# Performance work log

Measured on AMD Instinct MI355X. Metric: run time of the kernel, lower is better.

## Reference

```python
import jax, jax.numpy as jnp
import numpy as np

NUM_EMBEDDINGS = 4096
EMBEDDING_DIM = 256


def setup_inputs() -> dict:
    key = jax.random.key(0)
    k1, k2 = jax.random.split(key)
    # x: [B, C, H, W] latent feature map, C == embedding_dim
    x = jax.random.normal(k1, (4, EMBEDDING_DIM, 64, 64), dtype=jnp.float32)
    # codebook initialized uniform(-1/K, 1/K) as in the torch module
    emb = jax.random.uniform(
        k2, (NUM_EMBEDDINGS, EMBEDDING_DIM), dtype=jnp.float32,
        minval=-1.0 / NUM_EMBEDDINGS, maxval=1.0 / NUM_EMBEDDINGS)
    return {"x": x, "emb": emb}


def reference(x, emb):
    # x: [B, C, H, W] -> x_flat: [B, L, C] with L = H*W
    B, C = x.shape[0], x.shape[1]
    x_flat = x.reshape(B, C, -1).transpose(0, 2, 1)
    x_sq = jnp.sum(x_flat * x_flat, axis=2, keepdims=True)      # [B, L, 1]
    e_sq = jnp.sum(emb * emb, axis=1)                            # [K]
    dots = jnp.einsum('blc,kc->blk', x_flat, emb)                # [B, L, K]
    distances = x_sq + e_sq - 2.0 * dots
    closest_indices = jnp.argmin(distances, axis=2)              # [B, L]
    return closest_indices, distances
```

## Files before the change

### kernel.cpp

```cpp
#include <hip/hip_runtime.h>
#include <hip/hip_fp16.h>

#define BB 4
#define CC 256
#define LL 4096
#define MM 16384
#define KK 4096
#define MARGIN 1.0e-4f

typedef _Float16 half8 __attribute__((ext_vector_type(8)));
typedef _Float16 half4_ __attribute__((ext_vector_type(4)));
typedef float f32x4 __attribute__((ext_vector_type(4)));

#define GLOAD16(gp, lp) __builtin_amdgcn_global_load_lds( \
    (const __attribute__((address_space(1))) void*)(gp),  \
    (__attribute__((address_space(3))) void*)(lp), 16, 0, 0)

__global__ void vq_prep(const float* __restrict__ x, const float* __restrict__ emb,
                        _Float16* __restrict__ xh, float* __restrict__ xsq,
                        _Float16* __restrict__ eh, float* __restrict__ esq) {
  __shared__ float tl[32][260];
  const int t = threadIdx.x;
  if (blockIdx.x < 512) {
    const int b = blockIdx.x >> 7, l0 = (blockIdx.x & 127) * 32;
    const float* src = x + (size_t)b * CC * LL + l0;
#pragma unroll
    for (int it = 0; it < 32; ++it) {
      const int idx = it * 256 + t;
      const int c = idx >> 5, l = idx & 31;
      tl[l][c] = src[(size_t)c * LL + l];
    }
    __syncthreads();
#pragma unroll
    for (int it = 0; it < 4; ++it) {
      const int u = it * 256 + t;
      const int l = u >> 5, c8 = (u & 31) * 8;
      half8 h;
#pragma unroll
      for (int j = 0; j < 8; ++j) h[j] = (_Float16)tl[l][c8 + j];
      *(half8*)(xh + ((size_t)(b * LL + l0 + l)) * CC + c8) = h;
    }
    if (t < 32) {
      float S[2];
#pragma unroll
      for (int blk = 0; blk < 2; ++blk) {
        float v[16];
#pragma unroll
        for (int ln = 0; ln < 16; ++ln) {
          float q[8];
#pragma unroll
          for (int j = 0; j < 8; ++j) {
            const float xv = tl[t][blk * 128 + j * 16 + ln];
            q[j] = xv * xv;
          }
          v[ln] = ((q[0] + q[1]) + (q[2] + q[3])) + ((q[4] + q[5]) + (q[6] + q[7]));
        }
        float s1[8], s2[4], s3[2];
#pragma unroll
        for (int ln = 0; ln < 8; ++ln) s1[ln] = v[ln] + v[ln + 8];
#pragma unroll
        for (int ln = 0; ln < 4; ++ln) s2[ln] = s1[ln] + s1[ln + 4];
#pragma unroll
        for (int ln = 0; ln < 2; ++ln) s3[ln] = s2[ln] + s2[ln + 2];
        S[blk] = s3[0] + s3[1];
      }
      xsq[b * LL + l0 + t] = S[0] + S[1];
    }
  } else {
    const int lane = t & 63, w = t >> 6;
    const int q = (blockIdx.x - 512) * 4 + w;
    const float4 v = ((const float4*)(emb + (size_t)q * CC))[lane];
    float vv[4] = {v.x, v.y, v.z, v.w};
    _Float16 h[4];
#pragma unroll
    for (int i = 0; i < 4; ++i) h[i] = (_Float16)(vv[i] * 4096.0f);
    *(half4_*)(eh + (size_t)q * CC + lane * 4) = half4_{h[0], h[1], h[2], h[3]};
    if (lane == 0) {
      const float* pe = emb + (size_t)q * CC;
      float S[2];
#pragma unroll
      for (int blk = 0; blk < 2; ++blk) {
        float vt[16];
#pragma unroll
        for (int ln = 0; ln < 16; ++ln) {
          float qq[8];
#pragma unroll
          for (int j = 0; j < 8; ++j) {
            const float ev = pe[blk * 128 + j * 16 + ln];
            qq[j] = ev * ev;
          }
          vt[ln] = ((qq[0] + qq[1]) + (qq[2] + qq[3])) + ((qq[4] + qq[5]) + (qq[6] + qq[7]));
        }
        float s1[8], s2[4], s3[2];
#pragma unroll
        for (int ln = 0; ln < 8; ++ln) s1[ln] = vt[ln] + vt[ln + 8];
#pragma unroll
        for (int ln = 0; ln < 4; ++ln) s2[ln] = s1[ln] + s1[ln + 4];
#pragma unroll
        for (int ln = 0; ln < 2; ++ln) s3[ln] = s2[ln] + s2[ln + 2];
        S[blk] = s3[0] + s3[1];
      }
      esq[q] = S[0] + S[1];
    }
  }
}

__global__ __launch_bounds__(256) void vq_gemm(
    const _Float16* __restrict__ xh, const _Float16* __restrict__ eh,
    const float* __restrict__ xsq, const float* __restrict__ esq,
    float* __restrict__ out,
    float* __restrict__ ps1, int* __restrict__ pi1, float* __restrict__ ps2) {
  __shared__ __align__(16) char smem[49152];
  float* sOut = (float*)smem;

  const int t = threadIdx.x, lane = t & 63, wid = t >> 6;
  const int wm = wid >> 1, wn = wid & 1;
  const int m0 = blockIdx.x * 128, n0 = blockIdx.y * 128;
  const int lm = lane & 15, kb = lane >> 4;

  const int srow = lane >> 2;
  const int scol = (((lane & 3) ^ (srow & 3)) * 8);
  const int chunk0 = wid * 2, chunk1 = wid * 2 + 1;
  const int row0 = chunk0 * 16 + srow, row1 = chunk1 * 16 + srow;
  const int rg = (kb ^ (lm & 3)) * 8;

  float ev[4], xs4[4][4];
#pragma unroll
  for (int ni = 0; ni < 4; ++ni) ev[ni] = esq[n0 + wn * 64 + ni * 16 + lm];
#pragma unroll
  for (int mi = 0; mi < 4; ++mi)
#pragma unroll
    for (int r = 0; r < 4; ++r)
      xs4[mi][r] = xsq[m0 + wm * 64 + mi * 16 + kb * 4 + r];
  __builtin_amdgcn_sched_barrier(0);

#define SA(b) ((_Float16*)(smem + (b) * 16384))
#define SB(b) ((_Float16*)(smem + (b) * 16384 + 8192))
#define STAGE(ks, buf) do {                                                   \
    const int kc_ = (ks) * 32 + scol;                                         \
    GLOAD16(xh + (size_t)(m0 + row0) * CC + kc_, SA(buf) + chunk0 * 512);     \
    GLOAD16(eh + (size_t)(n0 + row0) * CC + kc_, SB(buf) + chunk0 * 512);     \
    GLOAD16(xh + (size_t)(m0 + row1) * CC + kc_, SA(buf) + chunk1 * 512);     \
    GLOAD16(eh + (size_t)(n0 + row1) * CC + kc_, SB(buf) + chunk1 * 512);     \
  } while (0)

  f32x4 acc[4][4] = {};
  STAGE(0, 0);
  STAGE(1, 1);
#pragma unroll
  for (int ks = 0; ks < 8; ++ks) {
    const int cur = ks % 3;
    if (ks < 7) {
      asm volatile("s_waitcnt vmcnt(4) lgkmcnt(0)" ::: "memory");
    } else {
      asm volatile("s_waitcnt vmcnt(0) lgkmcnt(0)" ::: "memory");
    }
    __builtin_amdgcn_s_barrier();
    __builtin_amdgcn_sched_barrier(0);

    if (ks < 6) STAGE(ks + 2, (ks + 2) % 3);

    half8 a[4], bfr[4];
#pragma unroll
    for (int i = 0; i < 4; ++i) {
      a[i]   = *(const half8*)&SA(cur)[(wm * 64 + i * 16 + lm) * 32 + rg];
      bfr[i] = *(const half8*)&SB(cur)[(wn * 64 + i * 16 + lm) * 32 + rg];
    }
#pragma unroll
    for (int mi = 0; mi < 4; ++mi)
#pragma unroll
      for (int ni = 0; ni < 4; ++ni)
        acc[mi][ni] = __builtin_amdgcn_mfma_f32_16x16x32_f16(a[mi], bfr[ni], acc[mi][ni], 0, 0, 0);
  }
#undef STAGE

#define EPI_BAR() do {                                          \
    asm volatile("s_waitcnt lgkmcnt(0)" ::: "memory");          \
    __builtin_amdgcn_s_barrier();                               \
    __builtin_amdgcn_sched_barrier(0);                          \
  } while (0)

  const int swz = kb << 4;
  const int erow = t >> 3, ej = t & 7;
  const int esw = ((erow >> 2) & 3) << 4;
  const int egm0 = m0 + (erow >> 4) * 64 + (erow & 15);

#pragma unroll
  for (int mi = 0; mi < 4; ++mi) {
#pragma unroll
    for (int r = 0; r < 4; ++r) {
      const int row = wm * 16 + kb * 4 + r;
#pragma unroll
      for (int ni = 0; ni < 4; ++ni) {
        float t1 = xs4[mi][r] + ev[ni];
        float d = t1 - acc[mi][ni][r] * 4.8828125e-4f;
        sOut[row * 128 + ((wn * 64 + ni * 16 + lm) ^ swz)] = d;
      }
    }
    EPI_BAR();
    float s1 = 3.4e38f, s2 = 3.4e38f;
    int q1 = 0x7fffffff;
    const int gm = egm0 + mi * 16;
#pragma unroll
    for (int i = 0; i < 4; ++i) {
      const int c = 4 * ej + 32 * i;
      const f32x4 v = *(const f32x4*)&sOut[erow * 128 + (c ^ esw)];
      __builtin_nontemporal_store(v, (f32x4*)(out + MM + (size_t)gm * (size_t)KK + n0 + c));
#pragma unroll
      for (int e = 0; e < 4; ++e) {
        const float d = v[e];
        const int q = n0 + c + e;
        if (d < s1 || (d == s1 && q < q1)) { s2 = s1; s1 = d; q1 = q; }
        else s2 = fminf(s2, d);
      }
    }
#pragma unroll
    for (int off = 1; off < 8; off <<= 1) {
      float o1 = __shfl_xor(s1, off), o2 = __shfl_xor(s2, off);
      int oq = __shfl_xor(q1, off);
      float mx = fmaxf(s1, o1);
      if (o1 < s1 || (o1 == s1 && oq < q1)) { s1 = o1; q1 = oq; }
      s2 = fminf(fminf(s2, o2), mx);
    }
    if (ej == 0) {
      const size_t pidx = (size_t)gm * 32 + blockIdx.y;
      ps1[pidx] = s1; pi1[pidx] = q1; ps2[pidx] = s2;
    }
    if (mi < 3) EPI_BAR();
  }
#undef EPI_BAR
#undef SA
#undef SB
}

__global__ void vq_finish(const float* __restrict__ ps1, const int* __restrict__ pi1,
                          const float* __restrict__ ps2, const float* __restrict__ dist,
                          const float* __restrict__ x, const float* __restrict__ emb,
                          const float* __restrict__ xsq, const float* __restrict__ esq,
                          float* __restrict__ out) {
  __shared__ float xr[4][CC];
  __shared__ int cq[4][64];
  __shared__ int cnt[4];
  const int lane = threadIdx.x & 63, w = threadIdx.x >> 6;
  const int m = blockIdx.x * 4 + w;

  float s1 = 3.4e38f, s2 = 3.4e38f;
  int q1 = 0x7fffffff;
  if (lane < 32) {
    const size_t base = (size_t)m * 32 + lane;
    s1 = ps1[base]; s2 = ps2[base]; q1 = pi1[base];
  }
#pragma unroll
  for (int off = 1; off < 32; off <<= 1) {
    float o1 = __shfl_xor(s1, off), o2 = __shfl_xor(s2, off);
    int oq = __shfl_xor(q1, off);
    float mx = fmaxf(s1, o1);
    if (o1 < s1 || (o1 == s1 && oq < q1)) { s1 = o1; q1 = oq; }
    s2 = fminf(fminf(s2, o2), mx);
  }
  s1 = __shfl(s1, 0); s2 = __shfl(s2, 0); q1 = __shfl(q1, 0);

  if (s2 - s1 > MARGIN) {
    if (lane == 0) out[m] = (float)q1;
    return;
  }

  const int b = m >> 12, l = m & 4095;
#pragma unroll
  for (int j = 0; j < 4; ++j)
    xr[w][lane * 4 + j] = x[((size_t)b * CC + lane * 4 + j) * LL + l];
  if (lane == 0) cnt[w] = 0;

  const float thr = s1 + MARGIN;
  const float4* d4 = (const float4*)(dist + (size_t)m * KK);
  for (int i = 0; i < 16; ++i) {
    float4 v = d4[i * 64 + lane];
    float vv[4] = {v.x, v.y, v.z, v.w};
#pragma unroll
    for (int e = 0; e < 4; ++e)
      if (vv[e] <= thr) {
        int slot = atomicAdd(&cnt[w], 1);
        if (slot < 64) cq[w][slot] = (i * 64 + lane) * 4 + e;
      }
  }
  const int nc = min(cnt[w], 64);
  float bs = 3.4e38f;
  int bq = 0x7fffffff;
  if (lane < nc) {
    const int q = cq[w][lane];
    const float* e = emb + (size_t)q * CC;
    float a = 0.f;
    for (int c = 0; c < CC; ++c) a = fmaf(xr[w][c], e[c], a);
    float t1 = xsq[m] + esq[q];
    bs = t1 - 2.0f * a;
    bq = q;
  }
#pragma unroll
  for (int off = 1; off < 64; off <<= 1) {
    float os = __shfl_xor(bs, off);
    int oq = __shfl_xor(bq, off);
    if (os < bs || (os == bs && oq < bq)) { bs = os; bq = oq; }
  }
  if (lane == 0) out[m] = (float)bq;
}

extern "C" void kernel_launch(void* const* d_in, const int* in_sizes, int n_in,
                              void* d_out, int out_size, void* d_ws, size_t ws_size,
                              hipStream_t stream) {
  const float* x = (const float*)d_in[0];
  const float* emb = (const float*)d_in[1];
  float* out = (float*)d_out;
  char* ws = (char*)d_ws;

  _Float16* xh = (_Float16*)(ws + 0);
  _Float16* eh = (_Float16*)(ws + 8388608);
  float* xsq = (float*)(ws + 10485760);
  float* esq = (float*)(ws + 10551296);
  float* ps1 = (float*)(ws + 10567680);
  int*   pi1 = (int*)(ws + 12664832);
  float* ps2 = (float*)(ws + 14761984);

  vq_prep<<<1536, 256, 0, stream>>>(x, emb, xh, xsq, eh, esq);
  vq_gemm<<<dim3(128, 32), 256, 0, stream>>>(xh, eh, xsq, esq, out, ps1, pi1, ps2);
  vq_finish<<<4096, 256, 0, stream>>>(ps1, pi1, ps2, out + MM, x, emb, xsq, esq, out);
}
```

Baseline: 127.4 us.

## Use per-wave LDS slices in GEMM epilogue to remove block barriers

The epilogue now has each wave stage its own 64x64 output quadrant in a private LDS slice, in two 32-row chunks. This replaces the block-wide tile that needed an s_barrier for every 16-row group. Each wave writes its distance rows and reduces top-2 minima over 64 columns, so the number of partial results per row doubles from 32 to 64. The finish kernel reads and reduces 64 partials per row with a full-wave shuffle reduction. This removes cross-wave synchronization, at the cost of more partial-result traffic and a longer shuffle chain.

```diff
diff --git a/kernel.cpp b/kernel.cpp
--- a/kernel.cpp
+++ b/kernel.cpp
@@ -111,7 +111,6 @@
     float* __restrict__ out,
     float* __restrict__ ps1, int* __restrict__ pi1, float* __restrict__ ps2) {
   __shared__ __align__(16) char smem[49152];
-  float* sOut = (float*)smem;
 
   const int t = threadIdx.x, lane = t & 63, wid = t >> 6;
   const int wm = wid >> 1, wn = wid & 1;
@@ -174,61 +173,66 @@
   }
 #undef STAGE
 
-#define EPI_BAR() do {                                          \
-    asm volatile("s_waitcnt lgkmcnt(0)" ::: "memory");          \
-    __builtin_amdgcn_s_barrier();                               \
-    __builtin_amdgcn_sched_barrier(0);                          \
-  } while (0)
-
+  asm volatile("s_waitcnt lgkmcnt(0)" ::: "memory");
+  __builtin_amdgcn_s_barrier();
+  __builtin_amdgcn_sched_barrier(0);
+
+  float* slice = (float*)(smem + wid * 8192);
   const int swz = kb << 4;
-  const int erow = t >> 3, ej = t & 7;
-  const int esw = ((erow >> 2) & 3) << 4;
-  const int egm0 = m0 + (erow >> 4) * 64 + (erow & 15);
-
-#pragma unroll
-  for (int mi = 0; mi < 4; ++mi) {
-#pragma unroll
-    for (int r = 0; r < 4; ++r) {
-      const int row = wm * 16 + kb * 4 + r;
-#pragma unroll
-      for (int ni = 0; ni < 4; ++ni) {
-        float t1 = xs4[mi][r] + ev[ni];
-        float d = t1 - acc[mi][ni][r] * 4.8828125e-4f;
-        sOut[row * 128 + ((wn * 64 + ni * 16 + lm) ^ swz)] = d;
-      }
-    }
-    EPI_BAR();
-    float s1 = 3.4e38f, s2 = 3.4e38f;
-    int q1 = 0x7fffffff;
-    const int gm = egm0 + mi * 16;
-#pragma unroll
-    for (int i = 0; i < 4; ++i) {
-      const int c = 4 * ej + 32 * i;
-      const f32x4 v = *(const f32x4*)&sOut[erow * 128 + (c ^ esw)];
-      __builtin_nontemporal_store(v, (f32x4*)(out + MM + (size_t)gm * (size_t)KK + n0 + c));
+
+#pragma unroll
+  for (int ch = 0; ch < 2; ++ch) {
+    if (ch) {
+      asm volatile("s_waitcnt lgkmcnt(0)" ::: "memory");
+      __builtin_amdgcn_sched_barrier(0);
+    }
+#pragma unroll
+    for (int mh = 0; mh < 2; ++mh) {
+      const int mi = ch * 2 + mh;
+#pragma unroll
+      for (int r = 0; r < 4; ++r) {
+        const int lr = mh * 16 + kb * 4 + r;
+#pragma unroll
+        for (int ni = 0; ni < 4; ++ni) {
+          float t1 = xs4[mi][r] + ev[ni];
+          float d = t1 - acc[mi][ni][r] * 4.8828125e-4f;
+          slice[lr * 64 + ((ni * 16 + lm) ^ swz)] = d;
+        }
+      }
+    }
+    asm volatile("s_waitcnt lgkmcnt(0)" ::: "memory");
+    __builtin_amdgcn_sched_barrier(0);
+#pragma unroll
+    for (int it = 0; it < 8; ++it) {
+      const int lr = it * 4 + kb;
+      const int c = lm * 4;
+      const f32x4 v = *(const f32x4*)&slice[lr * 64 + (c ^ ((it & 3) << 4))];
+      const int gm = m0 + wm * 64 + ch * 32 + lr;
+      __builtin_nontemporal_store(v,
+          (f32x4*)(out + MM + (size_t)gm * (size_t)KK + n0 + wn * 64 + c));
+      float s1 = 3.4e38f, s2 = 3.4e38f;
+      int q1 = 0x7fffffff;
 #pragma unroll
       for (int e = 0; e < 4; ++e) {
         const float d = v[e];
-        const int q = n0 + c + e;
+        const int q = n0 + wn * 64 + c + e;
         if (d < s1 || (d == s1 && q < q1)) { s2 = s1; s1 = d; q1 = q; }
         else s2 = fminf(s2, d);
       }
-    }
-#pragma unroll
-    for (int off = 1; off < 8; off <<= 1) {
-      float o1 = __shfl_xor(s1, off), o2 = __shfl_xor(s2, off);
-      int oq = __shfl_xor(q1, off);
-      float mx = fmaxf(s1, o1);
-      if (o1 < s1 || (o1 == s1 && oq < q1)) { s1 = o1; q1 = oq; }
-      s2 = fminf(fminf(s2, o2), mx);
-    }
-    if (ej == 0) {
-      const size_t pidx = (size_t)gm * 32 + blockIdx.y;
-      ps1[pidx] = s1; pi1[pidx] = q1; ps2[pidx] = s2;
-    }
-    if (mi < 3) EPI_BAR();
-  }
-#undef EPI_BAR
+#pragma unroll
+      for (int off = 1; off < 16; off <<= 1) {
+        float o1 = __shfl_xor(s1, off), o2 = __shfl_xor(s2, off);
+        int oq = __shfl_xor(q1, off);
+        float mx = fmaxf(s1, o1);
+        if (o1 < s1 || (o1 == s1 && oq < q1)) { s1 = o1; q1 = oq; }
+        s2 = fminf(fminf(s2, o2), mx);
+      }
+      if (lm == 0) {
+        const size_t pidx = (size_t)gm * 64 + blockIdx.y * 2 + wn;
+        ps1[pidx] = s1; pi1[pidx] = q1; ps2[pidx] = s2;
+      }
+    }
+  }
 #undef SA
 #undef SB
 }
@@ -244,21 +248,17 @@
   const int lane = threadIdx.x & 63, w = threadIdx.x >> 6;
   const int m = blockIdx.x * 4 + w;
 
-  float s1 = 3.4e38f, s2 = 3.4e38f;
-  int q1 = 0x7fffffff;
-  if (lane < 32) {
-    const size_t base = (size_t)m * 32 + lane;
-    s1 = ps1[base]; s2 = ps2[base]; q1 = pi1[base];
-  }
-#pragma unroll
-  for (int off = 1; off < 32; off <<= 1) {
+  const size_t base = (size_t)m * 64 + lane;
+  float s1 = ps1[base], s2 = ps2[base];
+  int q1 = pi1[base];
+#pragma unroll
+  for (int off = 1; off < 64; off <<= 1) {
     float o1 = __shfl_xor(s1, off), o2 = __shfl_xor(s2, off);
     int oq = __shfl_xor(q1, off);
     float mx = fmaxf(s1, o1);
     if (o1 < s1 || (o1 == s1 && oq < q1)) { s1 = o1; q1 = oq; }
     s2 = fminf(fminf(s2, o2), mx);
   }
-  s1 = __shfl(s1, 0); s2 = __shfl(s2, 0); q1 = __shfl(q1, 0);
 
   if (s2 - s1 > MARGIN) {
     if (lane == 0) out[m] = (float)q1;
@@ -317,8 +317,8 @@
   float* xsq = (float*)(ws + 10485760);
   float* esq = (float*)(ws + 10551296);
   float* ps1 = (float*)(ws + 10567680);
-  int*   pi1 = (int*)(ws + 12664832);
-  float* ps2 = (float*)(ws + 14761984);
+  int*   pi1 = (int*)(ws + 14761984);
+  float* ps2 = (float*)(ws + 18956288);
 
   vq_prep<<<1536, 256, 0, stream>>>(x, emb, xh, xsq, eh, esq);
   vq_gemm<<<dim3(128, 32), 256, 0, stream>>>(xh, eh, xsq, esq, out, ps1, pi1, ps2);
```

Measured after the change: 178.2 us. +39.9%, slower.
